# Kernel tuning notes

Hardware: AMD Instinct MI355X
Metric: run time of the kernel (lower is better)

The kernel has to match this reference:

```python
import jax, jax.numpy as jnp
import numpy as np

N_NODES = 100000
N_EDGES = 1000000
IN_F, HID_F, OUT_F = 64, 64, 32


def setup_inputs() -> dict:
    key = jax.random.key(0)
    k1, k2, k3, k4, k5, k6, k7 = jax.random.split(key, 7)
    x = jax.random.normal(k1, (N_NODES, IN_F), dtype=jnp.float32)
    src = jax.random.randint(k2, (N_EDGES,), 0, N_NODES, dtype=jnp.int32)
    dst = jax.random.randint(k3, (N_EDGES,), 0, N_NODES, dtype=jnp.int32)
    edge_index = jnp.stack([src, dst], axis=0)
    # Glorot-ish init for the two GraphConv weights + biases (DGL default has bias)
    W1 = jax.random.normal(k4, (IN_F, HID_F), dtype=jnp.float32) / np.sqrt(IN_F)
    b1 = jnp.zeros((HID_F,), dtype=jnp.float32)
    W2 = jax.random.normal(k5, (HID_F, OUT_F), dtype=jnp.float32) / np.sqrt(HID_F)
    b2 = jnp.zeros((OUT_F,), dtype=jnp.float32)
    return {"x": x, "edge_index": edge_index, "W1": W1, "b1": b1, "W2": W2, "b2": b2}


def reference(x, edge_index, W1, b1, W2, b2):
    src = edge_index[0]
    dst = edge_index[1]
    n = x.shape[0]
    ones = jnp.ones(src.shape[0], dtype=x.dtype)
    out_deg = jax.ops.segment_sum(ones, src, num_segments=n)  # out-degree of src nodes
    in_deg = jax.ops.segment_sum(ones, dst, num_segments=n)   # in-degree of dst nodes
    # DGL clamps degree to >= 1 before taking the -1/2 power (norm='both')
    norm_src = jnp.maximum(out_deg, 1.0) ** -0.5  # [N]
    norm_dst = jnp.maximum(in_deg, 1.0) ** -0.5   # [N]

    def graph_conv(h, W, b):
        # D_out^{-1/2} scaling on source side, aggregate, D_in^{-1/2} on dest side, then dense transform
        h = h * norm_src[:, None]
        agg = jax.ops.segment_sum(h[src], dst, num_segments=n)  # SpMM: sum over in-edges
        agg = agg * norm_dst[:, None]
        return agg @ W + b

    h = jax.nn.relu(graph_conv(x, W1, b1))
    return jax.nn.relu(graph_conv(h, W2, b2))
```

## Files before the change

kernel.cpp:

```cpp
#include <hip/hip_runtime.h>

#define IN_F 64
#define HID_F 64
#define OUT_F 32
#define BSH 8
#define BNODES 256
#define CAP 4096
#define NBMAX 400
#define CHUNK 4096

#define WAVE_BAR() __builtin_amdgcn_wave_barrier()

__global__ __launch_bounds__(256) void bin_kernel(
    const int* __restrict__ src, const int* __restrict__ dst,
    int* __restrict__ cursD, int* __restrict__ cursS,
    int2* __restrict__ dstBin, int* __restrict__ srcBin, int nE, int NB) {
    __shared__ int cntD[NBMAX], cntS[NBMAX], curD[NBMAX], curS[NBMAX];
    const int t = threadIdx.x;
    for (int i = t; i < NB; i += 256) { cntD[i] = 0; cntS[i] = 0; }
    __syncthreads();

    const int e0 = blockIdx.x * CHUNK;
    for (int k = t; k < CHUNK; k += 256) {
        int e = e0 + k;
        if (e < nE) {
            atomicAdd(&cntD[dst[e] >> BSH], 1);
            atomicAdd(&cntS[src[e] >> BSH], 1);
        }
    }
    __syncthreads();
    for (int i = t; i < NB; i += 256) {
        curD[i] = cntD[i] ? atomicAdd(&cursD[i], cntD[i]) : 0;
        curS[i] = cntS[i] ? atomicAdd(&cursS[i], cntS[i]) : 0;
    }
    __syncthreads();
    for (int k = t; k < CHUNK; k += 256) {
        int e = e0 + k;
        if (e < nE) {
            int s = src[e], d = dst[e];
            int pD = atomicAdd(&curD[d >> BSH], 1);
            if (pD < CAP) dstBin[(size_t)(d >> BSH) * CAP + pD] = make_int2(s, d);
            int pS = atomicAdd(&curS[s >> BSH], 1);
            if (pS < CAP) srcBin[(size_t)(s >> BSH) * CAP + pS] = s;
        }
    }
}

__global__ __launch_bounds__(256) void csr_bucket_kernel(
    const int2* __restrict__ dstBin, const int* __restrict__ cursD,
    int* __restrict__ row_ptr, int* __restrict__ deg, float* __restrict__ nd,
    int* __restrict__ csr_src, int n) {
    __shared__ int cnt[BNODES], cur[BNODES], lptr[BNODES], tmp[BNODES];
    const int b = blockIdx.x;
    const int t = threadIdx.x;
    const int node0 = b << BSH;
    int count = cursD[b]; if (count > CAP) count = CAP;
    cnt[t] = 0; cur[t] = 0;
    __syncthreads();
    const int2* bin = dstBin + (size_t)b * CAP;
    for (int e = t; e < count; e += 256) atomicAdd(&cnt[bin[e].y - node0], 1);
    __syncthreads();
    const int vv = cnt[t];
    tmp[t] = vv;
    __syncthreads();
    for (int off = 1; off < 256; off <<= 1) {
        int a = (t >= off) ? tmp[t - off] : 0;
        __syncthreads();
        tmp[t] += a;
        __syncthreads();
    }
    lptr[t] = tmp[t] - vv;
    __syncthreads();
    const int node = node0 + t;
    if (node < n) {
        row_ptr[node] = b * CAP + lptr[t];
        deg[node] = vv;
        nd[node] = rsqrtf(fmaxf((float)vv, 1.0f));
    }
    int* csr_b = csr_src + (size_t)b * CAP;
    for (int e = t; e < count; e += 256) {
        int2 p = bin[e];
        int l = p.y - node0;
        int r = atomicAdd(&cur[l], 1);
        csr_b[lptr[l] + r] = p.x;
    }
}

__global__ __launch_bounds__(256) void ns_bucket_kernel(
    const int* __restrict__ srcBin, const int* __restrict__ cursS,
    float* __restrict__ ns, int n) {
    __shared__ int cnt[BNODES];
    const int b = blockIdx.x;
    const int t = threadIdx.x;
    const int node0 = b << BSH;
    int count = cursS[b]; if (count > CAP) count = CAP;
    cnt[t] = 0;
    __syncthreads();
    const int* bin = srcBin + (size_t)b * CAP;
    for (int e = t; e < count; e += 256) atomicAdd(&cnt[bin[e] - node0], 1);
    __syncthreads();
    const int node = node0 + t;
    if (node < n) ns[node] = rsqrtf(fmaxf((float)cnt[t], 1.0f));
}

__global__ __launch_bounds__(256) void layer1_kernel(
    const float4* __restrict__ x4, const float* __restrict__ ns, const float* __restrict__ nd,
    const int* __restrict__ row_ptr, const int* __restrict__ deg,
    const int* __restrict__ csr_src,
    const float* __restrict__ W1, const float* __restrict__ b1,
    const float* __restrict__ W2, float* __restrict__ t2, int n) {
    __shared__ float W1l[64 * 64];
    __shared__ float W2l[64 * 32];
    __shared__ float rows[16][68];

    const int tid = threadIdx.x;
    for (int i = tid; i < 64 * 64; i += 256) W1l[i] = W1[i];
    for (int i = tid; i < 64 * 32; i += 256) W2l[i] = W2[i];
    __syncthreads();

    const int slot = tid >> 4;
    const int lane = tid & 15;
    float bj0 = b1[lane * 4 + 0], bj1 = b1[lane * 4 + 1];
    float bj2 = b1[lane * 4 + 2], bj3 = b1[lane * 4 + 3];

    const int ngroups = (n + 15) >> 4;
    for (int g = blockIdx.x; g < ngroups; g += gridDim.x) {
        const int node = g * 16 + slot;
        if (node >= n) continue;

        float4 a0 = {0, 0, 0, 0}, a1 = {0, 0, 0, 0}, a2 = {0, 0, 0, 0}, a3 = {0, 0, 0, 0};
        const int beg = row_ptr[node], end = beg + deg[node];
        int i = beg;
        for (; i + 4 <= end; i += 4) {
            int s0 = csr_src[i], s1 = csr_src[i + 1], s2 = csr_src[i + 2], s3 = csr_src[i + 3];
            float4 v0 = x4[(size_t)s0 * 16 + lane];
            float4 v1 = x4[(size_t)s1 * 16 + lane];
            float4 v2 = x4[(size_t)s2 * 16 + lane];
            float4 v3 = x4[(size_t)s3 * 16 + lane];
            float w0 = ns[s0], w1 = ns[s1], w2 = ns[s2], w3 = ns[s3];
            a0.x = fmaf(v0.x, w0, a0.x); a0.y = fmaf(v0.y, w0, a0.y);
            a0.z = fmaf(v0.z, w0, a0.z); a0.w = fmaf(v0.w, w0, a0.w);
            a1.x = fmaf(v1.x, w1, a1.x); a1.y = fmaf(v1.y, w1, a1.y);
            a1.z = fmaf(v1.z, w1, a1.z); a1.w = fmaf(v1.w, w1, a1.w);
            a2.x = fmaf(v2.x, w2, a2.x); a2.y = fmaf(v2.y, w2, a2.y);
            a2.z = fmaf(v2.z, w2, a2.z); a2.w = fmaf(v2.w, w2, a2.w);
            a3.x = fmaf(v3.x, w3, a3.x); a3.y = fmaf(v3.y, w3, a3.y);
            a3.z = fmaf(v3.z, w3, a3.z); a3.w = fmaf(v3.w, w3, a3.w);
        }
        for (; i < end; ++i) {
            int s = csr_src[i];
            float4 v = x4[(size_t)s * 16 + lane];
            float w = ns[s];
            a0.x = fmaf(v.x, w, a0.x); a0.y = fmaf(v.y, w, a0.y);
            a0.z = fmaf(v.z, w, a0.z); a0.w = fmaf(v.w, w, a0.w);
        }
        const float ndv = nd[node];
        float rx = (a0.x + a1.x + a2.x + a3.x) * ndv;
        float ry = (a0.y + a1.y + a2.y + a3.y) * ndv;
        float rz = (a0.z + a1.z + a2.z + a3.z) * ndv;
        float rw = (a0.w + a1.w + a2.w + a3.w) * ndv;

        WAVE_BAR();
        rows[slot][lane * 4 + 0] = rx;
        rows[slot][lane * 4 + 1] = ry;
        rows[slot][lane * 4 + 2] = rz;
        rows[slot][lane * 4 + 3] = rw;
        WAVE_BAR();

        float o0 = bj0, o1 = bj1, o2 = bj2, o3 = bj3;
#pragma unroll
        for (int k = 0; k < 64; ++k) {
            const float r = rows[slot][k];
            o0 = fmaf(r, W1l[k * 64 + lane * 4 + 0], o0);
            o1 = fmaf(r, W1l[k * 64 + lane * 4 + 1], o1);
            o2 = fmaf(r, W1l[k * 64 + lane * 4 + 2], o2);
            o3 = fmaf(r, W1l[k * 64 + lane * 4 + 3], o3);
        }
        const float nsv = ns[node];
        o0 = fmaxf(o0, 0.0f) * nsv; o1 = fmaxf(o1, 0.0f) * nsv;
        o2 = fmaxf(o2, 0.0f) * nsv; o3 = fmaxf(o3, 0.0f) * nsv;

        WAVE_BAR();
        rows[slot][lane * 4 + 0] = o0;
        rows[slot][lane * 4 + 1] = o1;
        rows[slot][lane * 4 + 2] = o2;
        rows[slot][lane * 4 + 3] = o3;
        WAVE_BAR();

        float p0 = 0.0f, p1 = 0.0f;
#pragma unroll
        for (int k = 0; k < 64; ++k) {
            const float r = rows[slot][k];
            p0 = fmaf(r, W2l[k * 32 + lane * 2 + 0], p0);
            p1 = fmaf(r, W2l[k * 32 + lane * 2 + 1], p1);
        }
        t2[(size_t)node * 32 + lane * 2 + 0] = p0;
        t2[(size_t)node * 32 + lane * 2 + 1] = p1;
    }
}

__global__ __launch_bounds__(256) void layer2_kernel(
    const float4* __restrict__ t24, const float* __restrict__ nd,
    const int* __restrict__ row_ptr, const int* __restrict__ deg,
    const int* __restrict__ csr_src,
    const float* __restrict__ b2, float4* __restrict__ out4, int n) {
    const int t = blockIdx.x * blockDim.x + threadIdx.x;
    const int node = t >> 3;
    const int lane = t & 7;
    if (node >= n) return;

    float4 a0 = {0, 0, 0, 0}, a1 = {0, 0, 0, 0}, a2 = {0, 0, 0, 0}, a3 = {0, 0, 0, 0};
    const int beg = row_ptr[node], end = beg + deg[node];
    int i = beg;
    for (; i + 4 <= end; i += 4) {
        int s0 = csr_src[i], s1 = csr_src[i + 1], s2 = csr_src[i + 2], s3 = csr_src[i + 3];
        float4 v0 = t24[(size_t)s0 * 8 + lane];
        float4 v1 = t24[(size_t)s1 * 8 + lane];
        float4 v2 = t24[(size_t)s2 * 8 + lane];
        float4 v3 = t24[(size_t)s3 * 8 + lane];
        a0.x += v0.x; a0.y += v0.y; a0.z += v0.z; a0.w += v0.w;
        a1.x += v1.x; a1.y += v1.y; a1.z += v1.z; a1.w += v1.w;
        a2.x += v2.x; a2.y += v2.y; a2.z += v2.z; a2.w += v2.w;
        a3.x += v3.x; a3.y += v3.y; a3.z += v3.z; a3.w += v3.w;
    }
    for (; i < end; ++i) {
        float4 v = t24[(size_t)csr_src[i] * 8 + lane];
        a0.x += v.x; a0.y += v.y; a0.z += v.z; a0.w += v.w;
    }
    const float ndv = nd[node];
    const float4 bb = ((const float4*)b2)[lane];
    float4 r;
    r.x = fmaxf(fmaf(a0.x + a1.x + a2.x + a3.x, ndv, bb.x), 0.0f);
    r.y = fmaxf(fmaf(a0.y + a1.y + a2.y + a3.y, ndv, bb.y), 0.0f);
    r.z = fmaxf(fmaf(a0.z + a1.z + a2.z + a3.z, ndv, bb.z), 0.0f);
    r.w = fmaxf(fmaf(a0.w + a1.w + a2.w + a3.w, ndv, bb.w), 0.0f);
    out4[(size_t)node * 8 + lane] = r;
}

extern "C" void kernel_launch(void* const* d_in, const int* in_sizes, int n_in,
                              void* d_out, int out_size, void* d_ws, size_t ws_size,
                              hipStream_t stream) {
    const float* x  = (const float*)d_in[0];
    const int* ei   = (const int*)d_in[1];
    const float* W1 = (const float*)d_in[2];
    const float* b1 = (const float*)d_in[3];
    const float* W2 = (const float*)d_in[4];
    const float* b2 = (const float*)d_in[5];
    float* out = (float*)d_out;

    const int n  = in_sizes[0] / IN_F;
    const int nE = in_sizes[1] / 2;
    const int* src = ei;
    const int* dst = ei + nE;
    const int NB = (n + BNODES - 1) >> BSH;

    int* cursD   = (int*)d_ws;
    int* cursS   = cursD + 512;
    int2* dstBin = (int2*)(cursS + 512);
    int* srcBin  = (int*)(dstBin + (size_t)NB * CAP);
    int* csr_src = srcBin + (size_t)NB * CAP;
    int* row_ptr = csr_src + (size_t)NB * CAP;
    int* deg     = row_ptr + n;
    float* ns    = (float*)(deg + n);
    float* nd    = ns + n;
    float* t2    = nd + n;

    hipMemsetAsync(d_ws, 0, 1024 * sizeof(int), stream);

    bin_kernel<<<(nE + CHUNK - 1) / CHUNK, 256, 0, stream>>>(
        src, dst, cursD, cursS, dstBin, srcBin, nE, NB);
    csr_bucket_kernel<<<NB, 256, 0, stream>>>(
        dstBin, cursD, row_ptr, deg, nd, csr_src, n);
    ns_bucket_kernel<<<NB, 256, 0, stream>>>(srcBin, cursS, ns, n);

    layer1_kernel<<<2048, 256, 0, stream>>>(
        (const float4*)x, ns, nd, row_ptr, deg, csr_src, W1, b1, W2, t2, n);
    layer2_kernel<<<(n * 8 + 255) / 256, 256, 0, stream>>>(
        (const float4*)t2, nd, row_ptr, deg, csr_src, b2, (float4*)out, n);
}
```

Baseline: 206.7 us.

## Gather FP16 pre-scaled features and FP16 hidden projections in both aggregation layers

Adds a prescale kernel that multiplies x by the source-degree normalization and stores it as FP16. Layer 1 then gathers these half-width rows without the per-edge ns lookup and multiply. Layer 1 also stores its projected hidden output t2 in FP16, which layer 2 gathers and widens to FP32 for accumulation. This halves the bytes moved by the random edge gathers in both layers. The cost is an extra elementwise pass over x and reduced precision in the gathered values.

Result: no change. 203.6 us (-1.5%).

```diff
diff --git a/kernel.cpp b/kernel.cpp
--- a/kernel.cpp
+++ b/kernel.cpp
@@ -1,4 +1,5 @@
 #include <hip/hip_runtime.h>
+#include <hip/hip_fp16.h>
 
 #define IN_F 64
 #define HID_F 64
@@ -10,6 +11,8 @@
 #define CHUNK 4096
 
 #define WAVE_BAR() __builtin_amdgcn_wave_barrier()
+
+union H2U { unsigned int u; __half h[2]; };
 
 __global__ __launch_bounds__(256) void bin_kernel(
     const int* __restrict__ src, const int* __restrict__ dst,
@@ -103,12 +106,26 @@
     if (node < n) ns[node] = rsqrtf(fmaxf((float)cnt[t], 1.0f));
 }
 
+__global__ __launch_bounds__(256) void prescale_kernel(
+    const float4* __restrict__ x4, const float* __restrict__ ns,
+    uint2* __restrict__ xh, int n) {
+    int i = blockIdx.x * blockDim.x + threadIdx.x;
+    if (i < n * 16) {
+        float s = ns[i >> 4];
+        float4 a = x4[i];
+        H2U lo, hi;
+        lo.h[0] = __float2half_rn(a.x * s); lo.h[1] = __float2half_rn(a.y * s);
+        hi.h[0] = __float2half_rn(a.z * s); hi.h[1] = __float2half_rn(a.w * s);
+        xh[i] = make_uint2(lo.u, hi.u);
+    }
+}
+
 __global__ __launch_bounds__(256) void layer1_kernel(
-    const float4* __restrict__ x4, const float* __restrict__ ns, const float* __restrict__ nd,
+    const uint2* __restrict__ xh, const float* __restrict__ ns, const float* __restrict__ nd,
     const int* __restrict__ row_ptr, const int* __restrict__ deg,
     const int* __restrict__ csr_src,
     const float* __restrict__ W1, const float* __restrict__ b1,
-    const float* __restrict__ W2, float* __restrict__ t2, int n) {
+    const float* __restrict__ W2, unsigned int* __restrict__ t2h, int n) {
     __shared__ float W1l[64 * 64];
     __shared__ float W2l[64 * 32];
     __shared__ float rows[16][68];
@@ -133,26 +150,25 @@
         int i = beg;
         for (; i + 4 <= end; i += 4) {
             int s0 = csr_src[i], s1 = csr_src[i + 1], s2 = csr_src[i + 2], s3 = csr_src[i + 3];
-            float4 v0 = x4[(size_t)s0 * 16 + lane];
-            float4 v1 = x4[(size_t)s1 * 16 + lane];
-            float4 v2 = x4[(size_t)s2 * 16 + lane];
-            float4 v3 = x4[(size_t)s3 * 16 + lane];
-            float w0 = ns[s0], w1 = ns[s1], w2 = ns[s2], w3 = ns[s3];
-            a0.x = fmaf(v0.x, w0, a0.x); a0.y = fmaf(v0.y, w0, a0.y);
-            a0.z = fmaf(v0.z, w0, a0.z); a0.w = fmaf(v0.w, w0, a0.w);
-            a1.x = fmaf(v1.x, w1, a1.x); a1.y = fmaf(v1.y, w1, a1.y);
-            a1.z = fmaf(v1.z, w1, a1.z); a1.w = fmaf(v1.w, w1, a1.w);
-            a2.x = fmaf(v2.x, w2, a2.x); a2.y = fmaf(v2.y, w2, a2.y);
-            a2.z = fmaf(v2.z, w2, a2.z); a2.w = fmaf(v2.w, w2, a2.w);
-            a3.x = fmaf(v3.x, w3, a3.x); a3.y = fmaf(v3.y, w3, a3.y);
-            a3.z = fmaf(v3.z, w3, a3.z); a3.w = fmaf(v3.w, w3, a3.w);
+            uint2 q0 = xh[(size_t)s0 * 16 + lane];
+            uint2 q1 = xh[(size_t)s1 * 16 + lane];
+            uint2 q2 = xh[(size_t)s2 * 16 + lane];
+            uint2 q3 = xh[(size_t)s3 * 16 + lane];
+            H2U c;
+            c.u = q0.x; a0.x += __half2float(c.h[0]); a0.y += __half2float(c.h[1]);
+            c.u = q0.y; a0.z += __half2float(c.h[0]); a0.w += __half2float(c.h[1]);
+            c.u = q1.x; a1.x += __half2float(c.h[0]); a1.y += __half2float(c.h[1]);
+            c.u = q1.y; a1.z += __half2float(c.h[0]); a1.w += __half2float(c.h[1]);
+            c.u = q2.x; a2.x += __half2float(c.h[0]); a2.y += __half2float(c.h[1]);
+            c.u = q2.y; a2.z += __half2float(c.h[0]); a2.w += __half2float(c.h[1]);
+            c.u = q3.x; a3.x += __half2float(c.h[0]); a3.y += __half2float(c.h[1]);
+            c.u = q3.y; a3.z += __half2float(c.h[0]); a3.w += __half2float(c.h[1]);
         }
         for (; i < end; ++i) {
-            int s = csr_src[i];
-            float4 v = x4[(size_t)s * 16 + lane];
-            float w = ns[s];
-            a0.x = fmaf(v.x, w, a0.x); a0.y = fmaf(v.y, w, a0.y);
-            a0.z = fmaf(v.z, w, a0.z); a0.w = fmaf(v.w, w, a0.w);
+            uint2 q = xh[(size_t)csr_src[i] * 16 + lane];
+            H2U c;
+            c.u = q.x; a0.x += __half2float(c.h[0]); a0.y += __half2float(c.h[1]);
+            c.u = q.y; a0.z += __half2float(c.h[0]); a0.w += __half2float(c.h[1]);
         }
         const float ndv = nd[node];
         float rx = (a0.x + a1.x + a2.x + a3.x) * ndv;
@@ -194,13 +210,15 @@
             p0 = fmaf(r, W2l[k * 32 + lane * 2 + 0], p0);
             p1 = fmaf(r, W2l[k * 32 + lane * 2 + 1], p1);
         }
-        t2[(size_t)node * 32 + lane * 2 + 0] = p0;
-        t2[(size_t)node * 32 + lane * 2 + 1] = p1;
+        H2U hp;
+        hp.h[0] = __float2half_rn(p0);
+        hp.h[1] = __float2half_rn(p1);
+        t2h[(size_t)node * 16 + lane] = hp.u;
     }
 }
 
 __global__ __launch_bounds__(256) void layer2_kernel(
-    const float4* __restrict__ t24, const float* __restrict__ nd,
+    const uint2* __restrict__ t2h, const float* __restrict__ nd,
     const int* __restrict__ row_ptr, const int* __restrict__ deg,
     const int* __restrict__ csr_src,
     const float* __restrict__ b2, float4* __restrict__ out4, int n) {
@@ -214,18 +232,25 @@
     int i = beg;
     for (; i + 4 <= end; i += 4) {
         int s0 = csr_src[i], s1 = csr_src[i + 1], s2 = csr_src[i + 2], s3 = csr_src[i + 3];
-        float4 v0 = t24[(size_t)s0 * 8 + lane];
-        float4 v1 = t24[(size_t)s1 * 8 + lane];
-        float4 v2 = t24[(size_t)s2 * 8 + lane];
-        float4 v3 = t24[(size_t)s3 * 8 + lane];
-        a0.x += v0.x; a0.y += v0.y; a0.z += v0.z; a0.w += v0.w;
-        a1.x += v1.x; a1.y += v1.y; a1.z += v1.z; a1.w += v1.w;
-        a2.x += v2.x; a2.y += v2.y; a2.z += v2.z; a2.w += v2.w;
-        a3.x += v3.x; a3.y += v3.y; a3.z += v3.z; a3.w += v3.w;
+        uint2 q0 = t2h[(size_t)s0 * 8 + lane];
+        uint2 q1 = t2h[(size_t)s1 * 8 + lane];
+        uint2 q2 = t2h[(size_t)s2 * 8 + lane];
+        uint2 q3 = t2h[(size_t)s3 * 8 + lane];
+        H2U c;
+        c.u = q0.x; a0.x += __half2float(c.h[0]); a0.y += __half2float(c.h[1]);
+        c.u = q0.y; a0.z += __half2float(c.h[0]); a0.w += __half2float(c.h[1]);
+        c.u = q1.x; a1.x += __half2float(c.h[0]); a1.y += __half2float(c.h[1]);
+        c.u = q1.y; a1.z += __half2float(c.h[0]); a1.w += __half2float(c.h[1]);
+        c.u = q2.x; a2.x += __half2float(c.h[0]); a2.y += __half2float(c.h[1]);
+        c.u = q2.y; a2.z += __half2float(c.h[0]); a2.w += __half2float(c.h[1]);
+        c.u = q3.x; a3.x += __half2float(c.h[0]); a3.y += __half2float(c.h[1]);
+        c.u = q3.y; a3.z += __half2float(c.h[0]); a3.w += __half2float(c.h[1]);
     }
     for (; i < end; ++i) {
-        float4 v = t24[(size_t)csr_src[i] * 8 + lane];
-        a0.x += v.x; a0.y += v.y; a0.z += v.z; a0.w += v.w;
+        uint2 q = t2h[(size_t)csr_src[i] * 8 + lane];
+        H2U c;
+        c.u = q.x; a0.x += __half2float(c.h[0]); a0.y += __half2float(c.h[1]);
+        c.u = q.y; a0.z += __half2float(c.h[0]); a0.w += __half2float(c.h[1]);
     }
     const float ndv = nd[node];
     const float4 bb = ((const float4*)b2)[lane];
@@ -263,7 +288,8 @@
     int* deg     = row_ptr + n;
     float* ns    = (float*)(deg + n);
     float* nd    = ns + n;
-    float* t2    = nd + n;
+    uint2* xh    = (uint2*)(nd + n);
+    unsigned int* t2h = (unsigned int*)(xh + (size_t)n * 16);
 
     hipMemsetAsync(d_ws, 0, 1024 * sizeof(int), stream);
 
@@ -272,9 +298,11 @@
     csr_bucket_kernel<<<NB, 256, 0, stream>>>(
         dstBin, cursD, row_ptr, deg, nd, csr_src, n);
     ns_bucket_kernel<<<NB, 256, 0, stream>>>(srcBin, cursS, ns, n);
+    prescale_kernel<<<(n * 16 + 255) / 256, 256, 0, stream>>>(
+        (const float4*)x, ns, xh, n);
 
     layer1_kernel<<<2048, 256, 0, stream>>>(
-        (const float4*)x, ns, nd, row_ptr, deg, csr_src, W1, b1, W2, t2, n);
+        xh, ns, nd, row_ptr, deg, csr_src, W1, b1, W2, t2h, n);
     layer2_kernel<<<(n * 8 + 255) / 256, 256, 0, stream>>>(
-        (const float4*)t2, nd, row_ptr, deg, csr_src, b2, (float4*)out, n);
-}
+        (const uint2*)t2h, nd, row_ptr, deg, csr_src, b2, (float4*)out, n);
+}
```
